# Performance work log

Measured on AMD Instinct MI355X. Metric: run time of the kernel, lower is better.

Reference implementation:

```python
import jax, jax.numpy as jnp
import numpy as np

H, D, HID, DIN = 2, 32, 64, 128
NQ, NA, NK = 100000, 200000, 200000
E_KQ, E_QK, E_QA, E_AQ = 800000, 800000, 400000, 400000
EP, EN = 100000, 100000


def setup_inputs() -> dict:
    key = jax.random.key(0)
    ks = jax.random.split(key, 32)
    f = lambda i, shape, s=0.05: jax.random.normal(ks[i], shape, dtype=jnp.float32) * s
    ri = lambda i, n, hi: jax.random.randint(ks[i], (n,), 0, hi)
    return {
        'xq': f(0, (NQ, DIN), 1.0), 'xa': f(1, (NA, DIN), 1.0), 'xk': f(2, (NK, DIN), 1.0),
        'lin_w': f(3, (3, DIN, HID)), 'lin_b': f(4, (3, HID)),
        'k_w': f(5, (3, HID, HID)), 'k_b': f(6, (3, HID)),
        'q_w': f(7, (3, HID, HID)), 'q_b': f(8, (3, HID)),
        'v_w': f(9, (3, HID, HID)), 'v_b': f(10, (3, HID)),
        'a_w': f(11, (3, HID, HID)), 'a_b': f(12, (3, HID)),
        'a_rel': f(13, (4, H, D, D), 0.2), 'm_rel': f(14, (4, H, D, D), 0.2),
        'p_rel': jnp.ones((4, H), dtype=jnp.float32),  # PyG init: ones
        'skip': jnp.ones((3,), dtype=jnp.float32),     # PyG init: ones
        'ei_kq_src': ri(15, E_KQ, NK), 'ei_kq_dst': ri(16, E_KQ, NQ),
        'ei_qk_src': ri(17, E_QK, NQ), 'ei_qk_dst': ri(18, E_QK, NA * 0 + NK),
        'ei_qa_src': ri(19, E_QA, NQ), 'ei_qa_dst': ri(20, E_QA, NA),
        'ei_aq_src': ri(21, E_AQ, NA), 'ei_aq_dst': ri(22, E_AQ, NQ),
        'pos_src': ri(23, EP, NQ), 'pos_dst': ri(24, EP, NA),
        'neg_src': ri(25, EN, NQ), 'neg_dst': ri(26, EN, NA),
    }


def _seg_softmax(alpha, dst, n):
    # softmax over incoming edges per destination node (per head)
    m = jax.ops.segment_max(alpha, dst, num_segments=n)
    m = jnp.where(jnp.isfinite(m), m, 0.0)
    e = jnp.exp(alpha - m[dst])
    s = jax.ops.segment_sum(e, dst, num_segments=n)
    return e / (s[dst] + 1e-16)


def hgt_forward(xq, xa, xk, lin_w, lin_b, k_w, k_b, q_w, q_b, v_w, v_b, a_w, a_b,
                a_rel, m_rel, p_rel, skip, edges):
    # node types: 0=question, 1=answer, 2=knowledge
    xs = [jax.nn.relu(x @ lin_w[i] + lin_b[i]) for i, x in enumerate([xq, xa, xk])]
    ns = [x.shape[0] for x in xs]
    k = [(x @ k_w[i] + k_b[i]).reshape(-1, H, D) for i, x in enumerate(xs)]
    q = [(x @ q_w[i] + q_b[i]).reshape(-1, H, D) for i, x in enumerate(xs)]
    v = [(x @ v_w[i] + v_b[i]).reshape(-1, H, D) for i, x in enumerate(xs)]
    out = [jnp.zeros((n, H, D), dtype=xs[0].dtype) for n in ns]
    scale = 1.0 / jnp.sqrt(jnp.float32(D))
    for st, dt, r, es, ed in edges:
        # per-edge-type head-wise key/value transforms (applied at node level)
        k_rel = jnp.einsum('nhd,hde->nhe', k[st], a_rel[r])
        v_rel = jnp.einsum('nhd,hde->nhe', v[st], m_rel[r])
        alpha = (q[dt][ed] * k_rel[es]).sum(-1) * p_rel[r] * scale  # [E,H]
        a = _seg_softmax(alpha, ed, ns[dt])
        msg = a[:, :, None] * v_rel[es]  # [E,H,D]
        out[dt] = out[dt] + jax.ops.segment_sum(msg, ed, num_segments=ns[dt])
    z = []
    for i in range(3):
        o = jax.nn.gelu(out[i].reshape(-1, H * D), approximate=False) @ a_w[i] + a_b[i]
        beta = jax.nn.sigmoid(skip[i])
        z.append(beta * o + (1.0 - beta) * xs[i])
    return z  # [z_question, z_answer, z_knowledge]; note: HGT.forward never applies self.lin


def reference(xq, xa, xk, lin_w, lin_b, k_w, k_b, q_w, q_b, v_w, v_b, a_w, a_b,
              a_rel, m_rel, p_rel, skip,
              ei_kq_src, ei_kq_dst, ei_qk_src, ei_qk_dst, ei_qa_src, ei_qa_dst,
              ei_aq_src, ei_aq_dst, pos_src, pos_dst, neg_src, neg_dst):
    edges = [
        (2, 0, 0, ei_kq_src, ei_kq_dst),  # knowledge -> question
        (0, 2, 1, ei_qk_src, ei_qk_dst),  # question -> knowledge
        (0, 1, 2, ei_qa_src, ei_qa_dst),  # question -> answer
        (1, 0, 3, ei_aq_src, ei_aq_dst),  # answer -> question
    ]
    zq, za, zk = hgt_forward(xq, xa, xk, lin_w, lin_b, k_w, k_b, q_w, q_b, v_w, v_b,
                             a_w, a_b, a_rel, m_rel, p_rel, skip, edges)
    pos_pred = jax.nn.sigmoid((zq[pos_src] * za[pos_dst]).sum(-1))
    neg_pred = jax.nn.sigmoid((zq[neg_src] * za[neg_dst]).sum(-1))
    return (pos_pred, neg_pred, zq, za, zk)
```

## Files before the change

### kernel.cpp

```cpp
#include <hip/hip_runtime.h>
#include <math.h>

namespace {

constexpr int NQn = 100000, NAn = 200000, NKn = 200000;
constexpr int EPc = 100000, ENc = 100000;
constexpr int ETOT = 2400000, NSEG = 600000;

constexpr long XSB_OFF  = 0;
constexpr long OUTB_OFF = 16000000;
constexpr long QBF_OFF  = 32000000;
constexpr long KV_OFF   = 48000000;
constexpr long ZB_OFF   = 86500000;
constexpr long WTB_OFF  = 96200000;
constexpr long WFB_OFF  = 96250000;
constexpr long INT_OFF  = 96300000;
constexpr long DEG_I  = 0;
constexpr long CUR_I  = 600000;
constexpr long OFFS_I = 1200000;
constexpr long PART_I = 1800064;
constexpr long CSRC_I = 1801088;

constexpr int LINT_U = 0;
constexpr int QT_U   = 24576;
constexpr int AT_U   = 36864;
constexpr int WFT_U  = 49152;

__constant__ long c_rbase[4] = {0, 200000, 300032, 400064};

typedef __attribute__((ext_vector_type(8))) short bf16x8;
typedef __attribute__((ext_vector_type(4))) float f32x4;

__device__ inline f32x4 mfma16(bf16x8 a, bf16x8 b, f32x4 c) {
    return __builtin_amdgcn_mfma_f32_16x16x32_bf16(a, b, c, 0, 0, 0);
}

__device__ inline float gelu_f(float x) {
    return 0.5f * x * (1.0f + erff(x * 0.7071067811865475f));
}
__device__ inline float bf2f(unsigned short u) {
    return __uint_as_float(((unsigned)u) << 16);
}
__device__ inline unsigned short f2bf(float f) {
    unsigned u = __float_as_uint(f);
    return (unsigned short)((u + 0x7fffu + ((u >> 16) & 1u)) >> 16);
}

__device__ inline void type_of_block128(int b, int& t, int& n0) {
    if (b < 782)       { t = 0; n0 = b * 128; }
    else if (b < 2345) { t = 1; n0 = (b - 782) * 128; }
    else               { t = 2; n0 = (b - 2345) * 128; }
}
__device__ inline void type_of_block64(int b, int& t, int& n0) {
    if (b < 1563)      { t = 0; n0 = b * 64; }
    else if (b < 4688) { t = 1; n0 = (b - 1563) * 64; }
    else               { t = 2; n0 = (b - 4688) * 64; }
}

template<int K>
__device__ inline void stage_bf16(unsigned short* lds, const unsigned short* src,
                                  int n0, int n, int tid)
{
    constexpr int CPR = K / 8;
    for (int c = tid; c < 128 * CPR; c += 256) {
        int row = c / CPR, kc = c % CPR;
        int node = n0 + row; if (node > n - 1) node = n - 1;
        uint4 v = *(const uint4*)&src[(long)node * K + kc * 8];
        int byte = (row * K + kc * 8) * 2;
        *(uint4*)((char*)lds + (byte ^ ((row & 7) << 4))) = v;
    }
}

__device__ inline void stage_out_gelu(unsigned short* lds, const unsigned short* src,
                                      int n0, int n, int tid)
{
    for (int c = tid; c < 128 * 8; c += 256) {
        int row = c >> 3, kc = c & 7;
        int node = n0 + row; if (node > n - 1) node = n - 1;
        uint4 v = *(const uint4*)&src[(long)node * 64 + kc * 8];
        float f0 = gelu_f(bf2f((unsigned short)(v.x & 0xffffu)));
        float f1 = gelu_f(bf2f((unsigned short)(v.x >> 16)));
        float f2 = gelu_f(bf2f((unsigned short)(v.y & 0xffffu)));
        float f3 = gelu_f(bf2f((unsigned short)(v.y >> 16)));
        float f4 = gelu_f(bf2f((unsigned short)(v.z & 0xffffu)));
        float f5 = gelu_f(bf2f((unsigned short)(v.z >> 16)));
        float f6 = gelu_f(bf2f((unsigned short)(v.w & 0xffffu)));
        float f7 = gelu_f(bf2f((unsigned short)(v.w >> 16)));
        uint4 o;
        o.x = (unsigned)f2bf(f0) | ((unsigned)f2bf(f1) << 16);
        o.y = (unsigned)f2bf(f2) | ((unsigned)f2bf(f3) << 16);
        o.z = (unsigned)f2bf(f4) | ((unsigned)f2bf(f5) << 16);
        o.w = (unsigned)f2bf(f6) | ((unsigned)f2bf(f7) << 16);
        int byte = (row * 64 + kc * 8) * 2;
        *(uint4*)((char*)lds + (byte ^ ((row & 7) << 4))) = o;
    }
}

template<int K, int ROWS>
__device__ inline void stage_f32(unsigned short* lds, const float* src,
                                 int n0, int n, int tid)
{
    constexpr int CPR = K / 8;
    for (int c = tid; c < ROWS * CPR; c += 256) {
        int row = c / CPR, kc = c % CPR;
        int node = n0 + row; if (node > n - 1) node = n - 1;
        const float* sp = &src[(long)node * K + kc * 8];
        float4 f0 = *(const float4*)sp, f1 = *(const float4*)(sp + 4);
        uint4 v;
        v.x = (unsigned)f2bf(f0.x) | ((unsigned)f2bf(f0.y) << 16);
        v.y = (unsigned)f2bf(f0.z) | ((unsigned)f2bf(f0.w) << 16);
        v.z = (unsigned)f2bf(f1.x) | ((unsigned)f2bf(f1.y) << 16);
        v.w = (unsigned)f2bf(f1.z) | ((unsigned)f2bf(f1.w) << 16);
        int byte = (row * K + kc * 8) * 2;
        *(uint4*)((char*)lds + (byte ^ ((row & 7) << 4))) = v;
    }
}

template<int N, int K>
__device__ inline void stage_w(unsigned short* lds, const unsigned short* wt, int tid)
{
    constexpr int CPR = K / 8;
    for (int c = tid; c < N * CPR; c += 256) {
        int nr = c / CPR, kc = c % CPR;
        uint4 v = *(const uint4*)&wt[nr * K + kc * 8];
        int byte = (nr * K + kc * 8) * 2;
        *(uint4*)((char*)lds + (byte ^ ((nr & 7) << 4))) = v;
    }
}

template<int K, int NF, int MF>
__device__ inline void mfma_coreT(const unsigned short* ldsX, const unsigned short* ldsW,
                                  f32x4 (&acc)[MF][NF], int lane, int w)
{
    const int lrow = lane & 15, lk = (lane >> 4) * 8;
    #pragma unroll
    for (int ks = 0; ks < K / 32; ++ks) {
        bf16x8 a[MF], b[NF];
        #pragma unroll
        for (int mf = 0; mf < MF; ++mf) {
            int row = w * (16 * MF) + mf * 16 + lrow;
            int byte = (row * K + ks * 32 + lk) * 2;
            a[mf] = *(const bf16x8*)((const char*)ldsX + (byte ^ ((row & 7) << 4)));
        }
        #pragma unroll
        for (int nf = 0; nf < NF; ++nf) {
            int nr = nf * 16 + lrow;
            int byte = (nr * K + ks * 32 + lk) * 2;
            b[nf] = *(const bf16x8*)((const char*)ldsW + (byte ^ ((nr & 7) << 4)));
        }
        #pragma unroll
        for (int mf = 0; mf < MF; ++mf)
            #pragma unroll
            for (int nf = 0; nf < NF; ++nf)
                acc[mf][nf] = mfma16(b[nf], a[mf], acc[mf][nf]);
    }
}

__global__ void prep_count(const float* __restrict__ lin_w, const float* __restrict__ q_w,
                           const float* __restrict__ a_w,
                           const float* __restrict__ kw, const float* __restrict__ kb,
                           const float* __restrict__ vw, const float* __restrict__ vb,
                           const float* __restrict__ a_rel, const float* __restrict__ m_rel,
                           unsigned short* __restrict__ wtb, float* __restrict__ wfb,
                           const int* __restrict__ d0, const int* __restrict__ d1,
                           const int* __restrict__ d2, const int* __restrict__ d3,
                           int* __restrict__ deg)
{
    const int tid = threadIdx.x;
    if (blockIdx.x < 4) {
        const int r = blockIdx.x;
        const int st_tab[4] = {2, 0, 0, 1};
        const int st = st_tab[r];
        for (int idx = tid; idx < 8192; idx += 256) {
            int d = idx >> 7, c = idx & 127;
            int i = c >> 1, which = c & 1;
            int h = i >> 5, e = i & 31;
            const float* w   = (which ? vw : kw) + st * 4096;
            const float* rel = (which ? m_rel : a_rel) + r * 2048;
            float s = 0.f;
            #pragma unroll
            for (int c32 = 0; c32 < 32; ++c32)
                s += w[d * 64 + h * 32 + c32] * rel[h * 1024 + c32 * 32 + e];
            wtb[WFT_U + r * 8192 + c * 64 + d] = f2bf(s);
        }
        for (int idx = tid; idx < 128; idx += 256) {
            int i = idx >> 1, which = idx & 1;
            int h = i >> 5, e = i & 31;
            const float* b   = (which ? vb : kb) + st * 64;
            const float* rel = (which ? m_rel : a_rel) + r * 2048;
            float s = 0.f;
            #pragma unroll
            for (int c32 = 0; c32 < 32; ++c32)
                s += b[h * 32 + c32] * rel[h * 1024 + c32 * 32 + e];
            wfb[r * 128 + idx] = s;
        }
    } else if (blockIdx.x < 196) {
        int i = (blockIdx.x - 4) * 256 + tid;
        if (i < 24576) {
            int t = i / 8192, rem = i % 8192, nn = rem >> 7, kk = rem & 127;
            wtb[LINT_U + i] = f2bf(lin_w[t * 8192 + kk * 64 + nn]);
        } else if (i < 36864) {
            int j = i - 24576;
            int t = j / 4096, rem = j % 4096, nn = rem >> 6, kk = rem & 63;
            wtb[QT_U + j] = f2bf(q_w[t * 4096 + kk * 64 + nn]);
        } else if (i < 49152) {
            int j = i - 36864;
            int t = j / 4096, rem = j % 4096, nn = rem >> 6, kk = rem & 63;
            wtb[AT_U + j] = f2bf(a_w[t * 4096 + kk * 64 + nn]);
        }
    } else {
        int gid = (blockIdx.x - 196) * 256 + tid;
        if (gid < 800000)       atomicAdd(&deg[d0[gid]], 1);
        else if (gid < 1600000) atomicAdd(&deg[100000 + d1[gid - 800000]], 1);
        else if (gid < 2000000) atomicAdd(&deg[300000 + d2[gid - 1600000]], 1);
        else if (gid < 2400000) atomicAdd(&deg[500000 + d3[gid - 2000000]], 1);
    }
}

__device__ inline void edge_map(int gid,
                                const int* __restrict__ s0, const int* __restrict__ d0,
                                const int* __restrict__ s1, const int* __restrict__ d1,
                                const int* __restrict__ s2, const int* __restrict__ d2,
                                const int* __restrict__ s3, const int* __restrict__ d3,
                                int& seg, int& s)
{
    if (gid < 800000)       { seg = d0[gid];                    s = s0[gid]; }
    else if (gid < 1600000) { seg = 100000 + d1[gid - 800000];  s = s1[gid - 800000]; }
    else if (gid < 2000000) { seg = 300000 + d2[gid - 1600000]; s = s2[gid - 1600000]; }
    else                    { seg = 500000 + d3[gid - 2000000]; s = s3[gid - 2000000]; }
}

__global__ void __launch_bounds__(256)
fill_lin(const int* __restrict__ s0, const int* __restrict__ d0,
         const int* __restrict__ s1, const int* __restrict__ d1,
         const int* __restrict__ s2, const int* __restrict__ d2,
         const int* __restrict__ s3, const int* __restrict__ d3,
         const int* __restrict__ off, int* __restrict__ cur, int* __restrict__ csrc,
         const float* __restrict__ xq, const float* __restrict__ xa,
         const float* __restrict__ xk, const unsigned short* __restrict__ wtb,
         const float* __restrict__ lin_b, unsigned short* __restrict__ xsb)
{
    __shared__ unsigned short ldsX[64 * 128];
    __shared__ unsigned short ldsW[64 * 128];
    const int b = blockIdx.x;
    const int tid = threadIdx.x;

    int linb, fillb;
    if (b < 9376) {
        if (b & 1) { fillb = b >> 1; linb = -1; }
        else       { linb = b >> 1;  fillb = -1; }
    } else { linb = 4688 + (b - 9376); fillb = -1; }

    if (fillb >= 0) {
        int base = fillb * 256 + tid;
        if (base < 1200000) {
            int segA, sA, segB, sB;
            edge_map(base,           s0, d0, s1, d1, s2, d2, s3, d3, segA, sA);
            edge_map(base + 1200000, s0, d0, s1, d1, s2, d2, s3, d3, segB, sB);
            int oA = off[segA], oB = off[segB];
            int slotA = oA + atomicAdd(&cur[segA], 1);
            int slotB = oB + atomicAdd(&cur[segB], 1);
            csrc[slotA] = sA;
            csrc[slotB] = sB;
        }
        return;
    }

    int t, n0; type_of_block64(linb, t, n0);
    const int cnt[3] = {NQn, NAn, NKn};
    const long noff[3] = {0, NQn, NQn + NAn};
    const float* X = (t == 0) ? xq : (t == 1) ? xa : xk;
    const int n = cnt[t];

    stage_w<64, 128>(ldsW, wtb + LINT_U + t * 8192, tid);
    stage_f32<128, 64>(ldsX, X, n0, n, tid);
    __syncthreads();

    const int w = tid >> 6, lane = tid & 63;
    f32x4 acc[1][4] = {};
    mfma_coreT<128, 4, 1>(ldsX, ldsW, acc, lane, w);

    const int nodeL = lane & 15, colG = (lane >> 4) * 4;
    int node = n0 + w * 16 + nodeL;
    if (node < n) {
        #pragma unroll
        for (int nf = 0; nf < 4; ++nf) {
            int col0 = nf * 16 + colG;
            float4 bv = *(const float4*)&lin_b[t * 64 + col0];
            ushort4 o;
            o.x = f2bf(fmaxf(acc[0][nf][0] + bv.x, 0.f));
            o.y = f2bf(fmaxf(acc[0][nf][1] + bv.y, 0.f));
            o.z = f2bf(fmaxf(acc[0][nf][2] + bv.z, 0.f));
            o.w = f2bf(fmaxf(acc[0][nf][3] + bv.w, 0.f));
            *(ushort4*)&xsb[(noff[t] + node) * 64 + col0] = o;
        }
    }
}

__global__ void __launch_bounds__(256)
qkv_split(const unsigned short* __restrict__ xsb, const unsigned short* __restrict__ wtb,
          const float* __restrict__ q_b, const float* __restrict__ wfb,
          unsigned short* __restrict__ qbf, unsigned short* __restrict__ kvb)
{
    __shared__ unsigned short ldsX[128 * 64];
    __shared__ unsigned short ldsW[128 * 64];
    const int cnt[3] = {NQn, NAn, NKn};
    const long noff[3] = {0, NQn, NQn + NAn};
    const int tid = threadIdx.x;
    const int w = tid >> 6, lane = tid & 63;
    const int nodeL = lane & 15, colG = (lane >> 4) * 4;
    const int b = blockIdx.x;

    if (b < 3908) {
        int t, n0; type_of_block128(b, t, n0);
        const int n = cnt[t];
        stage_bf16<64>(ldsX, xsb + noff[t] * 64, n0, n, tid);
        stage_w<64, 64>(ldsW, wtb + QT_U + t * 4096, tid);
        __syncthreads();

        f32x4 acc[2][4] = {};
        mfma_coreT<64, 4, 2>(ldsX, ldsW, acc, lane, w);
        #pragma unroll
        for (int mf = 0; mf < 2; ++mf) {
            int node = n0 + w * 32 + mf * 16 + nodeL;
            if (node < n) {
                #pragma unroll
                for (int nf = 0; nf < 4; ++nf) {
                    int col0 = nf * 16 + colG;
                    float4 bv = *(const float4*)&q_b[t * 64 + col0];
                    ushort4 o;
                    o.x = f2bf(acc[mf][nf][0] + bv.x);
                    o.y = f2bf(acc[mf][nf][1] + bv.y);
                    o.z = f2bf(acc[mf][nf][2] + bv.z);
                    o.w = f2bf(acc[mf][nf][3] + bv.w);
                    *(ushort4*)&qbf[(noff[t] + node) * 64 + col0] = o;
                }
            }
        }
    } else {
        int kb = b - 3908, r, lb;
        if (kb < 1563)      { r = 0; lb = kb; }
        else if (kb < 2345) { r = 1; lb = kb - 1563; }
        else if (kb < 3127) { r = 2; lb = kb - 2345; }
        else                { r = 3; lb = kb - 3127; }
        const int stt[4] = {2, 0, 0, 1};
        const int st = stt[r];
        const int n0 = lb * 128;
        const int n = cnt[st];
        const long rb = c_rbase[r];

        stage_bf16<64>(ldsX, xsb + noff[st] * 64, n0, n, tid);
        stage_w<128, 64>(ldsW, wtb + WFT_U + r * 8192, tid);
        __syncthreads();

        f32x4 acc[2][8] = {};
        mfma_coreT<64, 8, 2>(ldsX, ldsW, acc, lane, w);
        #pragma unroll
        for (int mf = 0; mf < 2; ++mf) {
            int node = n0 + w * 32 + mf * 16 + nodeL;
            if (node < n) {
                #pragma unroll
                for (int nf = 0; nf < 8; ++nf) {
                    int col0 = nf * 16 + colG;
                    float4 bv = *(const float4*)&wfb[r * 128 + col0];
                    ushort4 o;
                    o.x = f2bf(acc[mf][nf][0] + bv.x);
                    o.y = f2bf(acc[mf][nf][1] + bv.y);
                    o.z = f2bf(acc[mf][nf][2] + bv.z);
                    o.w = f2bf(acc[mf][nf][3] + bv.w);
                    *(ushort4*)&kvb[(rb + node) * 128 + col0] = o;
                }
            }
        }
    }
}

__global__ void __launch_bounds__(256)
head_mfma(const unsigned short* __restrict__ outb, const unsigned short* __restrict__ xsb,
          const unsigned short* __restrict__ wtb, const float* __restrict__ a_b,
          const float* __restrict__ skip, float* __restrict__ z,
          unsigned short* __restrict__ zb)
{
    __shared__ unsigned short ldsX[128 * 64];
    __shared__ unsigned short ldsW[64 * 64];
    int t, n0; type_of_block128(blockIdx.x, t, n0);
    const int cnt[3] = {NQn, NAn, NKn};
    const long noff[3] = {0, NQn, NQn + NAn};
    const long zoff[3] = {200000L, 6600000L, 19400000L};
    const int n = cnt[t];
    const int tid = threadIdx.x;

    stage_w<64, 64>(ldsW, wtb + AT_U + t * 4096, tid);
    stage_out_gelu(ldsX, outb + noff[t] * 64, n0, n, tid);
    __syncthreads();

    const int w = tid >> 6, lane = tid & 63;
    f32x4 acc[2][4] = {};
    mfma_coreT<64, 4, 2>(ldsX, ldsW, acc, lane, w);

    const float beta = 1.f / (1.f + expf(-skip[t]));
    const int nodeL = lane & 15, colG = (lane >> 4) * 4;
    #pragma unroll
    for (int mf = 0; mf < 2; ++mf) {
        int node = n0 + w * 32 + mf * 16 + nodeL;
        if (node < n) {
            #pragma unroll
            for (int nf = 0; nf < 4; ++nf) {
                int col0 = nf * 16 + colG;
                float4 bv = *(const float4*)&a_b[t * 64 + col0];
                ushort4 rv = *(const ushort4*)&xsb[(noff[t] + node) * 64 + col0];
                float4 o;
                o.x = beta * (acc[mf][nf][0] + bv.x) + (1.f - beta) * bf2f(rv.x);
                o.y = beta * (acc[mf][nf][1] + bv.y) + (1.f - beta) * bf2f(rv.y);
                o.z = beta * (acc[mf][nf][2] + bv.z) + (1.f - beta) * bf2f(rv.z);
                o.w = beta * (acc[mf][nf][3] + bv.w) + (1.f - beta) * bf2f(rv.w);
                *(float4*)&z[zoff[t] + (long)node * 64 + col0] = o;
                if (t < 2) {
                    ushort4 p;
                    p.x = f2bf(o.x); p.y = f2bf(o.y); p.z = f2bf(o.z); p.w = f2bf(o.w);
                    long zrow = (t == 0) ? (long)node : 100000L + node;
                    *(ushort4*)&zb[zrow * 64 + col0] = p;
                }
            }
        }
    }
}

__global__ void scan1(const int* __restrict__ in, int* __restrict__ out,
                      int* __restrict__ part, int n)
{
    __shared__ int lds[256];
    const int tid = threadIdx.x;
    const int base = blockIdx.x * 1024 + tid * 4;
    int v[4];
    #pragma unroll
    for (int k = 0; k < 4; ++k) v[k] = (base + k < n) ? in[base + k] : 0;
    int tsum = v[0] + v[1] + v[2] + v[3];
    lds[tid] = tsum;
    __syncthreads();
    for (int off = 1; off < 256; off <<= 1) {
        int t = (tid >= off) ? lds[tid - off] : 0;
        __syncthreads();
        lds[tid] += t;
        __syncthreads();
    }
    int excl = lds[tid] - tsum;
    #pragma unroll
    for (int k = 0; k < 4; ++k) {
        if (base + k < n) out[base + k] = excl;
        excl += v[k];
    }
    if (tid == 255) part[blockIdx.x] = lds[255];
}

__global__ void scan2(int* __restrict__ part, int nb)
{
    __shared__ int lds[256];
    const int tid = threadIdx.x;
    const int base = tid * 4;
    int v[4];
    #pragma unroll
    for (int k = 0; k < 4; ++k) v[k] = (base + k < nb) ? part[base + k] : 0;
    int tsum = v[0] + v[1] + v[2] + v[3];
    lds[tid] = tsum;
    __syncthreads();
    for (int off = 1; off < 256; off <<= 1) {
        int t = (tid >= off) ? lds[tid - off] : 0;
        __syncthreads();
        lds[tid] += t;
        __syncthreads();
    }
    int excl = lds[tid] - tsum;
    #pragma unroll
    for (int k = 0; k < 4; ++k) {
        if (base + k < nb) part[base + k] = excl;
        excl += v[k];
    }
}

__global__ void scan3(int* __restrict__ off, const int* __restrict__ part, int n, int E)
{
    int i = blockIdx.x * 256 + threadIdx.x;
    if (i < n) off[i] += part[i >> 10];
    if (i == 0) off[n] = E;
}

__device__ inline void attn_node(const int* __restrict__ csrc, int begin, int end,
                                 const unsigned short* __restrict__ kvt,
                                 const float qv[4], int j, float res[4])
{
    float ss = 0.f, a0 = 0.f, a1 = 0.f, a2 = 0.f, a3 = 0.f;

    for (int t = begin; t < end; t += 4) {
        bool v1 = (t + 1 < end), v2 = (t + 2 < end), v3 = (t + 3 < end);
        int s0 = csrc[t];
        int s1 = csrc[v1 ? t + 1 : t];
        int s2 = csrc[v2 ? t + 2 : t];
        int s3 = csrc[v3 ? t + 3 : t];
        uint4 k0 = *(const uint4*)(kvt + (long)s0 * 128 + j * 8);
        uint4 k1 = *(const uint4*)(kvt + (long)s1 * 128 + j * 8);
        uint4 k2 = *(const uint4*)(kvt + (long)s2 * 128 + j * 8);
        uint4 k3 = *(const uint4*)(kvt + (long)s3 * 128 + j * 8);

        float p0 = __uint_as_float(k0.x << 16) * qv[0] + __uint_as_float(k0.y << 16) * qv[1]
                 + __uint_as_float(k0.z << 16) * qv[2] + __uint_as_float(k0.w << 16) * qv[3];
        float p1 = __uint_as_float(k1.x << 16) * qv[0] + __uint_as_float(k1.y << 16) * qv[1]
                 + __uint_as_float(k1.z << 16) * qv[2] + __uint_as_float(k1.w << 16) * qv[3];
        float p2 = __uint_as_float(k2.x << 16) * qv[0] + __uint_as_float(k2.y << 16) * qv[1]
                 + __uint_as_float(k2.z << 16) * qv[2] + __uint_as_float(k2.w << 16) * qv[3];
        float p3 = __uint_as_float(k3.x << 16) * qv[0] + __uint_as_float(k3.y << 16) * qv[1]
                 + __uint_as_float(k3.z << 16) * qv[2] + __uint_as_float(k3.w << 16) * qv[3];

        p0 += __shfl_xor(p0, 1);  p1 += __shfl_xor(p1, 1);
        p2 += __shfl_xor(p2, 1);  p3 += __shfl_xor(p3, 1);
        p0 += __shfl_xor(p0, 2);  p1 += __shfl_xor(p1, 2);
        p2 += __shfl_xor(p2, 2);  p3 += __shfl_xor(p3, 2);
        p0 += __shfl_xor(p0, 4);  p1 += __shfl_xor(p1, 4);
        p2 += __shfl_xor(p2, 4);  p3 += __shfl_xor(p3, 4);

        float w0 = exp2f(fminf(p0, 115.f));
        float w1 = v1 ? exp2f(fminf(p1, 115.f)) : 0.f;
        float w2 = v2 ? exp2f(fminf(p2, 115.f)) : 0.f;
        float w3 = v3 ? exp2f(fminf(p3, 115.f)) : 0.f;

        ss += (w0 + w1) + (w2 + w3);
        a0 += w0 * __uint_as_float(k0.x & 0xffff0000u) + w1 * __uint_as_float(k1.x & 0xffff0000u)
            + w2 * __uint_as_float(k2.x & 0xffff0000u) + w3 * __uint_as_float(k3.x & 0xffff0000u);
        a1 += w0 * __uint_as_float(k0.y & 0xffff0000u) + w1 * __uint_as_float(k1.y & 0xffff0000u)
            + w2 * __uint_as_float(k2.y & 0xffff0000u) + w3 * __uint_as_float(k3.y & 0xffff0000u);
        a2 += w0 * __uint_as_float(k0.z & 0xffff0000u) + w1 * __uint_as_float(k1.z & 0xffff0000u)
            + w2 * __uint_as_float(k2.z & 0xffff0000u) + w3 * __uint_as_float(k3.z & 0xffff0000u);
        a3 += w0 * __uint_as_float(k0.w & 0xffff0000u) + w1 * __uint_as_float(k1.w & 0xffff0000u)
            + w2 * __uint_as_float(k2.w & 0xffff0000u) + w3 * __uint_as_float(k3.w & 0xffff0000u);
    }

    float inv = 1.f / (ss + 1e-16f);
    res[0] = a0 * inv; res[1] = a1 * inv; res[2] = a2 * inv; res[3] = a3 * inv;
}

__global__ void __launch_bounds__(256)
attn_all(const int* __restrict__ off, const int* __restrict__ csrc,
         const unsigned short* __restrict__ qbf, const unsigned short* __restrict__ kv,
         const float* __restrict__ prel, float scale, unsigned short* __restrict__ outb)
{
    const int tid = threadIdx.x;
    const int nid = blockIdx.x * 16 + (tid >> 4);
    const int j = tid & 15;
    const int h = j >> 3;
    const float l2e = 1.4426950408889634f;

    long row; int segA, segB = -1; long kbA, kbB = 0; float psA, psB = 0.f;
    if (nid < 100000) {
        row = nid;
        segA = nid;            kbA = c_rbase[0]; psA = prel[0 + h] * scale * l2e;
        segB = 500000 + nid;   kbB = c_rbase[3]; psB = prel[6 + h] * scale * l2e;
    } else if (nid < 300000) {
        int kk = nid - 100000;
        row = 300000 + kk;
        segA = 100000 + kk;    kbA = c_rbase[1]; psA = prel[2 + h] * scale * l2e;
    } else {
        int aa = nid - 300000;
        row = 100000 + aa;
        segA = 300000 + aa;    kbA = c_rbase[2]; psA = prel[4 + h] * scale * l2e;
    }

    ushort4 q4 = *(const ushort4*)&qbf[row * 64 + 4 * j];
    float qraw[4] = {bf2f(q4.x), bf2f(q4.y), bf2f(q4.z), bf2f(q4.w)};

    float res[4];
    {
        float qv[4] = {qraw[0] * psA, qraw[1] * psA, qraw[2] * psA, qraw[3] * psA};
        attn_node(csrc, off[segA], off[segA + 1], kv + kbA * 128, qv, j, res);
    }
    if (segB >= 0) {
        float qv[4] = {qraw[0] * psB, qraw[1] * psB, qraw[2] * psB, qraw[3] * psB};
        float r2[4];
        attn_node(csrc, off[segB], off[segB + 1], kv + kbB * 128, qv, j, r2);
        res[0] += r2[0]; res[1] += r2[1]; res[2] += r2[2]; res[3] += r2[3];
    }

    ushort4 o;
    o.x = f2bf(res[0]); o.y = f2bf(res[1]); o.z = f2bf(res[2]); o.w = f2bf(res[3]);
    *(ushort4*)&outb[row * 64 + 4 * j] = o;
}

__global__ void pred_all(const int* __restrict__ psrc, const int* __restrict__ pdst,
                         const int* __restrict__ nsrc, const int* __restrict__ ndst,
                         const unsigned short* __restrict__ zb, float* __restrict__ out)
{
    int t = blockIdx.x * 256 + threadIdx.x;
    int g = t >> 3, lane = t & 7;
    if (g >= EPc + ENc) return;
    int s, d;
    if (g < EPc) { s = psrc[g]; d = pdst[g]; }
    else         { int gg = g - EPc; s = nsrc[gg]; d = ndst[gg]; }
    uint4 zs = *(const uint4*)&zb[(long)s * 64 + lane * 8];
    uint4 zd = *(const uint4*)&zb[(100000L + d) * 64 + lane * 8];
    float p = 0.f;
    p += bf2f((unsigned short)(zs.x & 0xffffu)) * bf2f((unsigned short)(zd.x & 0xffffu));
    p += bf2f((unsigned short)(zs.x >> 16))     * bf2f((unsigned short)(zd.x >> 16));
    p += bf2f((unsigned short)(zs.y & 0xffffu)) * bf2f((unsigned short)(zd.y & 0xffffu));
    p += bf2f((unsigned short)(zs.y >> 16))     * bf2f((unsigned short)(zd.y >> 16));
    p += bf2f((unsigned short)(zs.z & 0xffffu)) * bf2f((unsigned short)(zd.z & 0xffffu));
    p += bf2f((unsigned short)(zs.z >> 16))     * bf2f((unsigned short)(zd.z >> 16));
    p += bf2f((unsigned short)(zs.w & 0xffffu)) * bf2f((unsigned short)(zd.w & 0xffffu));
    p += bf2f((unsigned short)(zs.w >> 16))     * bf2f((unsigned short)(zd.w >> 16));
    p += __shfl_xor(p, 1);
    p += __shfl_xor(p, 2);
    p += __shfl_xor(p, 4);
    if (lane == 0) out[g] = 1.f / (1.f + expf(-p));
}

}

extern "C" void kernel_launch(void* const* d_in, const int* in_sizes, int n_in,
                              void* d_out, int out_size, void* d_ws, size_t ws_size,
                              hipStream_t stream)
{
    const float* xq    = (const float*)d_in[0];
    const float* xa    = (const float*)d_in[1];
    const float* xk    = (const float*)d_in[2];
    const float* lin_w = (const float*)d_in[3];
    const float* lin_b = (const float*)d_in[4];
    const float* k_w   = (const float*)d_in[5];
    const float* k_b   = (const float*)d_in[6];
    const float* q_w   = (const float*)d_in[7];
    const float* q_b   = (const float*)d_in[8];
    const float* v_w   = (const float*)d_in[9];
    const float* v_b   = (const float*)d_in[10];
    const float* a_w   = (const float*)d_in[11];
    const float* a_b   = (const float*)d_in[12];
    const float* a_rel = (const float*)d_in[13];
    const float* m_rel = (const float*)d_in[14];
    const float* p_rel = (const float*)d_in[15];
    const float* skip  = (const float*)d_in[16];
    const int* esrc[4] = {(const int*)d_in[17], (const int*)d_in[19], (const int*)d_in[21], (const int*)d_in[23]};
    const int* edst[4] = {(const int*)d_in[18], (const int*)d_in[20], (const int*)d_in[22], (const int*)d_in[24]};
    const int* pos_src = (const int*)d_in[25];
    const int* pos_dst = (const int*)d_in[26];
    const int* neg_src = (const int*)d_in[27];
    const int* neg_dst = (const int*)d_in[28];

    float* ws   = (float*)d_ws;
    float* outp = (float*)d_out;
    int*   wi   = (int*)(ws + INT_OFF);
    unsigned short* xsb  = (unsigned short*)(ws + XSB_OFF);
    unsigned short* outb = (unsigned short*)(ws + OUTB_OFF);
    unsigned short* qbf  = (unsigned short*)(ws + QBF_OFF);
    unsigned short* kvb  = (unsigned short*)(ws + KV_OFF);
    unsigned short* zbb  = (unsigned short*)(ws + ZB_OFF);
    unsigned short* wtb  = (unsigned short*)(ws + WTB_OFF);
    float*          wfb  = ws + WFB_OFF;

    hipMemsetAsync(wi + DEG_I, 0, 1200000L * sizeof(int), stream);

    prep_count<<<196 + 9375, 256, 0, stream>>>(
        lin_w, q_w, a_w, k_w, k_b, v_w, v_b, a_rel, m_rel, wtb, wfb,
        edst[0], edst[1], edst[2], edst[3], wi + DEG_I);

    const int nb = (NSEG + 1023) / 1024;
    scan1<<<nb, 256, 0, stream>>>(wi + DEG_I, wi + OFFS_I, wi + PART_I, NSEG);
    scan2<<<1, 256, 0, stream>>>(wi + PART_I, nb);
    scan3<<<(NSEG + 255) / 256, 256, 0, stream>>>(wi + OFFS_I, wi + PART_I, NSEG, ETOT);

    fill_lin<<<12501, 256, 0, stream>>>(
        esrc[0], edst[0], esrc[1], edst[1], esrc[2], edst[2], esrc[3], edst[3],
        wi + OFFS_I, wi + CUR_I, wi + CSRC_I,
        xq, xa, xk, wtb, lin_b, xsb);

    qkv_split<<<8598, 256, 0, stream>>>(xsb, wtb, q_b, wfb, qbf, kvb);

    const float scale = 0.17677669529663687f;
    attn_all<<<31250, 256, 0, stream>>>(wi + OFFS_I, wi + CSRC_I, qbf, kvb,
                                        p_rel, scale, outb);

    head_mfma<<<3908, 256, 0, stream>>>(outb, xsb, wtb, a_b, skip, outp, zbb);

    pred_all<<<(200000 * 8 + 255) / 256, 256, 0, stream>>>(
        pos_src, pos_dst, neg_src, neg_dst, zbb, outp);
}
```

Measured before the change: 594.1 us.

## Move input linear into prep/degree-count kernel and merge QKV with CSR fill

The input projection (linear+ReLU) now runs inside the first kernel alongside weight prep and degree counting, and stages lin_w directly from fp32 with an in-LDS transpose instead of using a pre-converted bf16 copy. The CSR fill is now interleaved with the QKV projection blocks in one launch, removing one kernel launch and letting the gather-heavy fill overlap with compute. The cost is that every linear block converts lin_w itself with scalar LDS stores, and block scheduling and occupancy now depend on how the mixed workloads share each launch.

Result: slower. 635.2 us (+6.9%).

```diff
diff --git a/kernel.cpp b/kernel.cpp
--- a/kernel.cpp
+++ b/kernel.cpp
@@ -21,10 +21,9 @@
 constexpr long PART_I = 1800064;
 constexpr long CSRC_I = 1801088;
 
-constexpr int LINT_U = 0;
-constexpr int QT_U   = 24576;
-constexpr int AT_U   = 36864;
-constexpr int WFT_U  = 49152;
+constexpr int QT_U   = 0;
+constexpr int AT_U   = 12288;
+constexpr int WFT_U  = 24576;
 
 __constant__ long c_rbase[4] = {0, 200000, 300032, 400064};
 
@@ -128,6 +127,21 @@
     }
 }
 
+__device__ inline void stage_wT_f32(unsigned short* lds, const float* w, int tid)
+{
+    for (int c = tid * 4; c < 8192; c += 1024) {
+        int kk = c >> 6, nn0 = c & 63;
+        float4 v = *(const float4*)&w[kk * 64 + nn0];
+        float vals[4] = {v.x, v.y, v.z, v.w};
+        #pragma unroll
+        for (int i = 0; i < 4; ++i) {
+            int nn = nn0 + i;
+            int byte = (nn * 128 + kk) * 2;
+            *(unsigned short*)((char*)lds + (byte ^ ((nn & 7) << 4))) = f2bf(vals[i]);
+        }
+    }
+}
+
 template<int K, int NF, int MF>
 __device__ inline void mfma_coreT(const unsigned short* ldsX, const unsigned short* ldsW,
                                   f32x4 (&acc)[MF][NF], int lane, int w)
@@ -156,19 +170,69 @@
     }
 }
 
-__global__ void prep_count(const float* __restrict__ lin_w, const float* __restrict__ q_w,
-                           const float* __restrict__ a_w,
-                           const float* __restrict__ kw, const float* __restrict__ kb,
-                           const float* __restrict__ vw, const float* __restrict__ vb,
-                           const float* __restrict__ a_rel, const float* __restrict__ m_rel,
-                           unsigned short* __restrict__ wtb, float* __restrict__ wfb,
-                           const int* __restrict__ d0, const int* __restrict__ d1,
-                           const int* __restrict__ d2, const int* __restrict__ d3,
-                           int* __restrict__ deg)
-{
+__device__ inline void edge_map(int gid,
+                                const int* __restrict__ s0, const int* __restrict__ d0,
+                                const int* __restrict__ s1, const int* __restrict__ d1,
+                                const int* __restrict__ s2, const int* __restrict__ d2,
+                                const int* __restrict__ s3, const int* __restrict__ d3,
+                                int& seg, int& s)
+{
+    if (gid < 800000)       { seg = d0[gid];                    s = s0[gid]; }
+    else if (gid < 1600000) { seg = 100000 + d1[gid - 800000];  s = s1[gid - 800000]; }
+    else if (gid < 2000000) { seg = 300000 + d2[gid - 1600000]; s = s2[gid - 1600000]; }
+    else                    { seg = 500000 + d3[gid - 2000000]; s = s3[gid - 2000000]; }
+}
+
+__global__ void __launch_bounds__(256)
+lin_prep_count(const float* __restrict__ xq, const float* __restrict__ xa,
+               const float* __restrict__ xk, const float* __restrict__ lin_w,
+               const float* __restrict__ lin_b, unsigned short* __restrict__ xsb,
+               const float* __restrict__ q_w, const float* __restrict__ a_w,
+               const float* __restrict__ kw, const float* __restrict__ kb,
+               const float* __restrict__ vw, const float* __restrict__ vb,
+               const float* __restrict__ a_rel, const float* __restrict__ m_rel,
+               unsigned short* __restrict__ wtb, float* __restrict__ wfb,
+               const int* __restrict__ d0, const int* __restrict__ d1,
+               const int* __restrict__ d2, const int* __restrict__ d3,
+               int* __restrict__ deg)
+{
+    __shared__ unsigned short ldsX[64 * 128];
+    __shared__ unsigned short ldsW[64 * 128];
+    const int b = blockIdx.x;
     const int tid = threadIdx.x;
-    if (blockIdx.x < 4) {
-        const int r = blockIdx.x;
+
+    if (b < 7813) {
+        int t, n0; type_of_block64(b, t, n0);
+        const int cnt[3] = {NQn, NAn, NKn};
+        const long noff[3] = {0, NQn, NQn + NAn};
+        const float* X = (t == 0) ? xq : (t == 1) ? xa : xk;
+        const int n = cnt[t];
+
+        stage_wT_f32(ldsW, lin_w + (long)t * 8192, tid);
+        stage_f32<128, 64>(ldsX, X, n0, n, tid);
+        __syncthreads();
+
+        const int w = tid >> 6, lane = tid & 63;
+        f32x4 acc[1][4] = {};
+        mfma_coreT<128, 4, 1>(ldsX, ldsW, acc, lane, w);
+
+        const int nodeL = lane & 15, colG = (lane >> 4) * 4;
+        int node = n0 + w * 16 + nodeL;
+        if (node < n) {
+            #pragma unroll
+            for (int nf = 0; nf < 4; ++nf) {
+                int col0 = nf * 16 + colG;
+                float4 bv = *(const float4*)&lin_b[t * 64 + col0];
+                ushort4 o;
+                o.x = f2bf(fmaxf(acc[0][nf][0] + bv.x, 0.f));
+                o.y = f2bf(fmaxf(acc[0][nf][1] + bv.y, 0.f));
+                o.z = f2bf(fmaxf(acc[0][nf][2] + bv.z, 0.f));
+                o.w = f2bf(fmaxf(acc[0][nf][3] + bv.w, 0.f));
+                *(ushort4*)&xsb[(noff[t] + node) * 64 + col0] = o;
+            }
+        }
+    } else if (b < 7817) {
+        const int r = b - 7813;
         const int st_tab[4] = {2, 0, 0, 1};
         const int st = st_tab[r];
         for (int idx = tid; idx < 8192; idx += 256) {
@@ -186,30 +250,26 @@
         for (int idx = tid; idx < 128; idx += 256) {
             int i = idx >> 1, which = idx & 1;
             int h = i >> 5, e = i & 31;
-            const float* b   = (which ? vb : kb) + st * 64;
+            const float* bb  = (which ? vb : kb) + st * 64;
             const float* rel = (which ? m_rel : a_rel) + r * 2048;
             float s = 0.f;
             #pragma unroll
             for (int c32 = 0; c32 < 32; ++c32)
-                s += b[h * 32 + c32] * rel[h * 1024 + c32 * 32 + e];
+                s += bb[h * 32 + c32] * rel[h * 1024 + c32 * 32 + e];
             wfb[r * 128 + idx] = s;
         }
-    } else if (blockIdx.x < 196) {
-        int i = (blockIdx.x - 4) * 256 + tid;
-        if (i < 24576) {
-            int t = i / 8192, rem = i % 8192, nn = rem >> 7, kk = rem & 127;
-            wtb[LINT_U + i] = f2bf(lin_w[t * 8192 + kk * 64 + nn]);
-        } else if (i < 36864) {
-            int j = i - 24576;
-            int t = j / 4096, rem = j % 4096, nn = rem >> 6, kk = rem & 63;
-            wtb[QT_U + j] = f2bf(q_w[t * 4096 + kk * 64 + nn]);
-        } else if (i < 49152) {
-            int j = i - 36864;
+    } else if (b < 7913) {
+        int i = (b - 7817) * 256 + tid;
+        if (i < 12288) {
+            int t = i / 4096, rem = i % 4096, nn = rem >> 6, kk = rem & 63;
+            wtb[QT_U + i] = f2bf(q_w[t * 4096 + kk * 64 + nn]);
+        } else {
+            int j = i - 12288;
             int t = j / 4096, rem = j % 4096, nn = rem >> 6, kk = rem & 63;
             wtb[AT_U + j] = f2bf(a_w[t * 4096 + kk * 64 + nn]);
         }
     } else {
-        int gid = (blockIdx.x - 196) * 256 + tid;
+        int gid = (b - 7913) * 256 + tid;
         if (gid < 800000)       atomicAdd(&deg[d0[gid]], 1);
         else if (gid < 1600000) atomicAdd(&deg[100000 + d1[gid - 800000]], 1);
         else if (gid < 2000000) atomicAdd(&deg[300000 + d2[gid - 1600000]], 1);
@@ -217,39 +277,26 @@
     }
 }
 
-__device__ inline void edge_map(int gid,
-                                const int* __restrict__ s0, const int* __restrict__ d0,
-                                const int* __restrict__ s1, const int* __restrict__ d1,
-                                const int* __restrict__ s2, const int* __restrict__ d2,
-                                const int* __restrict__ s3, const int* __restrict__ d3,
-                                int& seg, int& s)
-{
-    if (gid < 800000)       { seg = d0[gid];                    s = s0[gid]; }
-    else if (gid < 1600000) { seg = 100000 + d1[gid - 800000];  s = s1[gid - 800000]; }
-    else if (gid < 2000000) { seg = 300000 + d2[gid - 1600000]; s = s2[gid - 1600000]; }
-    else                    { seg = 500000 + d3[gid - 2000000]; s = s3[gid - 2000000]; }
-}
-
 __global__ void __launch_bounds__(256)
-fill_lin(const int* __restrict__ s0, const int* __restrict__ d0,
+fill_qkv(const int* __restrict__ s0, const int* __restrict__ d0,
          const int* __restrict__ s1, const int* __restrict__ d1,
          const int* __restrict__ s2, const int* __restrict__ d2,
          const int* __restrict__ s3, const int* __restrict__ d3,
          const int* __restrict__ off, int* __restrict__ cur, int* __restrict__ csrc,
-         const float* __restrict__ xq, const float* __restrict__ xa,
-         const float* __restrict__ xk, const unsigned short* __restrict__ wtb,
-         const float* __restrict__ lin_b, unsigned short* __restrict__ xsb)
-{
-    __shared__ unsigned short ldsX[64 * 128];
-    __shared__ unsigned short ldsW[64 * 128];
+         const unsigned short* __restrict__ xsb, const unsigned short* __restrict__ wtb,
+         const float* __restrict__ q_b, const float* __restrict__ wfb,
+         unsigned short* __restrict__ qbf, unsigned short* __restrict__ kvb)
+{
+    __shared__ unsigned short ldsX[128 * 64];
+    __shared__ unsigned short ldsW[128 * 64];
     const int b = blockIdx.x;
     const int tid = threadIdx.x;
 
-    int linb, fillb;
+    int qkvb, fillb;
     if (b < 9376) {
-        if (b & 1) { fillb = b >> 1; linb = -1; }
-        else       { linb = b >> 1;  fillb = -1; }
-    } else { linb = 4688 + (b - 9376); fillb = -1; }
+        if (b & 1) { fillb = b >> 1; qkvb = -1; }
+        else       { qkvb = b >> 1;  fillb = -1; }
+    } else { qkvb = 4688 + (b - 9376); fillb = -1; }
 
     if (fillb >= 0) {
         int base = fillb * 256 + tid;
@@ -266,53 +313,13 @@
         return;
     }
 
-    int t, n0; type_of_block64(linb, t, n0);
     const int cnt[3] = {NQn, NAn, NKn};
     const long noff[3] = {0, NQn, NQn + NAn};
-    const float* X = (t == 0) ? xq : (t == 1) ? xa : xk;
-    const int n = cnt[t];
-
-    stage_w<64, 128>(ldsW, wtb + LINT_U + t * 8192, tid);
-    stage_f32<128, 64>(ldsX, X, n0, n, tid);
-    __syncthreads();
-
-    const int w = tid >> 6, lane = tid & 63;
-    f32x4 acc[1][4] = {};
-    mfma_coreT<128, 4, 1>(ldsX, ldsW, acc, lane, w);
-
-    const int nodeL = lane & 15, colG = (lane >> 4) * 4;
-    int node = n0 + w * 16 + nodeL;
-    if (node < n) {
-        #pragma unroll
-        for (int nf = 0; nf < 4; ++nf) {
-            int col0 = nf * 16 + colG;
-            float4 bv = *(const float4*)&lin_b[t * 64 + col0];
-            ushort4 o;
-            o.x = f2bf(fmaxf(acc[0][nf][0] + bv.x, 0.f));
-            o.y = f2bf(fmaxf(acc[0][nf][1] + bv.y, 0.f));
-            o.z = f2bf(fmaxf(acc[0][nf][2] + bv.z, 0.f));
-            o.w = f2bf(fmaxf(acc[0][nf][3] + bv.w, 0.f));
-            *(ushort4*)&xsb[(noff[t] + node) * 64 + col0] = o;
-        }
-    }
-}
-
-__global__ void __launch_bounds__(256)
-qkv_split(const unsigned short* __restrict__ xsb, const unsigned short* __restrict__ wtb,
-          const float* __restrict__ q_b, const float* __restrict__ wfb,
-          unsigned short* __restrict__ qbf, unsigned short* __restrict__ kvb)
-{
-    __shared__ unsigned short ldsX[128 * 64];
-    __shared__ unsigned short ldsW[128 * 64];
-    const int cnt[3] = {NQn, NAn, NKn};
-    const long noff[3] = {0, NQn, NQn + NAn};
-    const int tid = threadIdx.x;
     const int w = tid >> 6, lane = tid & 63;
     const int nodeL = lane & 15, colG = (lane >> 4) * 4;
-    const int b = blockIdx.x;
-
-    if (b < 3908) {
-        int t, n0; type_of_block128(b, t, n0);
+
+    if (qkvb < 3908) {
+        int t, n0; type_of_block128(qkvb, t, n0);
         const int n = cnt[t];
         stage_bf16<64>(ldsX, xsb + noff[t] * 64, n0, n, tid);
         stage_w<64, 64>(ldsW, wtb + QT_U + t * 4096, tid);
@@ -338,7 +345,7 @@
             }
         }
     } else {
-        int kb = b - 3908, r, lb;
+        int kb = qkvb - 3908, r, lb;
         if (kb < 1563)      { r = 0; lb = kb; }
         else if (kb < 2345) { r = 1; lb = kb - 1563; }
         else if (kb < 3127) { r = 2; lb = kb - 2345; }
@@ -654,8 +661,9 @@
 
     hipMemsetAsync(wi + DEG_I, 0, 1200000L * sizeof(int), stream);
 
-    prep_count<<<196 + 9375, 256, 0, stream>>>(
-        lin_w, q_w, a_w, k_w, k_b, v_w, v_b, a_rel, m_rel, wtb, wfb,
+    lin_prep_count<<<7913 + 9375, 256, 0, stream>>>(
+        xq, xa, xk, lin_w, lin_b, xsb,
+        q_w, a_w, k_w, k_b, v_w, v_b, a_rel, m_rel, wtb, wfb,
         edst[0], edst[1], edst[2], edst[3], wi + DEG_I);
 
     const int nb = (NSEG + 1023) / 1024;
@@ -663,12 +671,10 @@
     scan2<<<1, 256, 0, stream>>>(wi + PART_I, nb);
     scan3<<<(NSEG + 255) / 256, 256, 0, stream>>>(wi + OFFS_I, wi + PART_I, NSEG, ETOT);
 
-    fill_lin<<<12501, 256, 0, stream>>>(
+    fill_qkv<<<13286, 256, 0, stream>>>(
         esrc[0], edst[0], esrc[1], edst[1], esrc[2], edst[2], esrc[3], edst[3],
         wi + OFFS_I, wi + CUR_I, wi + CSRC_I,
-        xq, xa, xk, wtb, lin_b, xsb);
-
-    qkv_split<<<8598, 256, 0, stream>>>(xsb, wtb, q_b, wfb, qbf, kvb);
+        xsb, wtb, q_b, wfb, qbf, kvb);
 
     const float scale = 0.17677669529663687f;
     attn_all<<<31250, 256, 0, stream>>>(wi + OFFS_I, wi + CSRC_I, qbf, kvb,
```

## Record per-edge rank during degree count to drop second atomic pass in CSR fill

Applied to the files above, without the earlier changes.

The degree-counting kernel now stores the value returned by each atomicAdd as that edge's rank within its destination segment. The CSR fill can then write each source index directly to offset plus rank, with no second atomic pass over a cursor array. The fill work is folded into every linear-projection block (two edges per thread) instead of alternating separate fill blocks, which shrinks the grid. This costs an extra 2.4M-int rank array that must be written and read back, but removes the cursor memset and the atomic contention in the fill. CSR order within a segment is now fixed by the count pass, so the sum order in the segment softmax can differ slightly.

Result: faster. 549.0 us (-7.6%).

```diff
diff --git a/kernel.cpp b/kernel.cpp
--- a/kernel.cpp
+++ b/kernel.cpp
@@ -6,6 +6,7 @@
 constexpr int NQn = 100000, NAn = 200000, NKn = 200000;
 constexpr int EPc = 100000, ENc = 100000;
 constexpr int ETOT = 2400000, NSEG = 600000;
+constexpr int LIN_THREADS = 7813 * 256;
 
 constexpr long XSB_OFF  = 0;
 constexpr long OUTB_OFF = 16000000;
@@ -16,10 +17,10 @@
 constexpr long WFB_OFF  = 96250000;
 constexpr long INT_OFF  = 96300000;
 constexpr long DEG_I  = 0;
-constexpr long CUR_I  = 600000;
-constexpr long OFFS_I = 1200000;
-constexpr long PART_I = 1800064;
-constexpr long CSRC_I = 1801088;
+constexpr long OFFS_I = 600064;
+constexpr long PART_I = 1200128;
+constexpr long RANK_I = 1201152;
+constexpr long CSRC_I = 3601152;
 
 constexpr int LINT_U = 0;
 constexpr int QT_U   = 24576;
@@ -156,6 +157,28 @@
     }
 }
 
+__device__ inline void edge_map(int gid,
+                                const int* __restrict__ s0, const int* __restrict__ d0,
+                                const int* __restrict__ s1, const int* __restrict__ d1,
+                                const int* __restrict__ s2, const int* __restrict__ d2,
+                                const int* __restrict__ s3, const int* __restrict__ d3,
+                                int& seg, int& s)
+{
+    if (gid < 800000)       { seg = d0[gid];                    s = s0[gid]; }
+    else if (gid < 1600000) { seg = 100000 + d1[gid - 800000];  s = s1[gid - 800000]; }
+    else if (gid < 2000000) { seg = 300000 + d2[gid - 1600000]; s = s2[gid - 1600000]; }
+    else                    { seg = 500000 + d3[gid - 2000000]; s = s3[gid - 2000000]; }
+}
+__device__ inline int edge_seg(int gid,
+                               const int* __restrict__ d0, const int* __restrict__ d1,
+                               const int* __restrict__ d2, const int* __restrict__ d3)
+{
+    if (gid < 800000)       return d0[gid];
+    else if (gid < 1600000) return 100000 + d1[gid - 800000];
+    else if (gid < 2000000) return 300000 + d2[gid - 1600000];
+    else                    return 500000 + d3[gid - 2000000];
+}
+
 __global__ void prep_count(const float* __restrict__ lin_w, const float* __restrict__ q_w,
                            const float* __restrict__ a_w,
                            const float* __restrict__ kw, const float* __restrict__ kb,
@@ -164,7 +187,7 @@
                            unsigned short* __restrict__ wtb, float* __restrict__ wfb,
                            const int* __restrict__ d0, const int* __restrict__ d1,
                            const int* __restrict__ d2, const int* __restrict__ d3,
-                           int* __restrict__ deg)
+                           int* __restrict__ deg, int* __restrict__ rank)
 {
     const int tid = threadIdx.x;
     if (blockIdx.x < 4) {
@@ -210,63 +233,43 @@
         }
     } else {
         int gid = (blockIdx.x - 196) * 256 + tid;
-        if (gid < 800000)       atomicAdd(&deg[d0[gid]], 1);
-        else if (gid < 1600000) atomicAdd(&deg[100000 + d1[gid - 800000]], 1);
-        else if (gid < 2000000) atomicAdd(&deg[300000 + d2[gid - 1600000]], 1);
-        else if (gid < 2400000) atomicAdd(&deg[500000 + d3[gid - 2000000]], 1);
-    }
-}
-
-__device__ inline void edge_map(int gid,
-                                const int* __restrict__ s0, const int* __restrict__ d0,
-                                const int* __restrict__ s1, const int* __restrict__ d1,
-                                const int* __restrict__ s2, const int* __restrict__ d2,
-                                const int* __restrict__ s3, const int* __restrict__ d3,
-                                int& seg, int& s)
-{
-    if (gid < 800000)       { seg = d0[gid];                    s = s0[gid]; }
-    else if (gid < 1600000) { seg = 100000 + d1[gid - 800000];  s = s1[gid - 800000]; }
-    else if (gid < 2000000) { seg = 300000 + d2[gid - 1600000]; s = s2[gid - 1600000]; }
-    else                    { seg = 500000 + d3[gid - 2000000]; s = s3[gid - 2000000]; }
+        if (gid < ETOT) {
+            int seg = edge_seg(gid, d0, d1, d2, d3);
+            rank[gid] = atomicAdd(&deg[seg], 1);
+        }
+    }
 }
 
 __global__ void __launch_bounds__(256)
-fill_lin(const int* __restrict__ s0, const int* __restrict__ d0,
+lin_fill(const int* __restrict__ s0, const int* __restrict__ d0,
          const int* __restrict__ s1, const int* __restrict__ d1,
          const int* __restrict__ s2, const int* __restrict__ d2,
          const int* __restrict__ s3, const int* __restrict__ d3,
-         const int* __restrict__ off, int* __restrict__ cur, int* __restrict__ csrc,
+         const int* __restrict__ off, const int* __restrict__ rank,
+         int* __restrict__ csrc,
          const float* __restrict__ xq, const float* __restrict__ xa,
          const float* __restrict__ xk, const unsigned short* __restrict__ wtb,
          const float* __restrict__ lin_b, unsigned short* __restrict__ xsb)
 {
     __shared__ unsigned short ldsX[64 * 128];
     __shared__ unsigned short ldsW[64 * 128];
-    const int b = blockIdx.x;
     const int tid = threadIdx.x;
-
-    int linb, fillb;
-    if (b < 9376) {
-        if (b & 1) { fillb = b >> 1; linb = -1; }
-        else       { linb = b >> 1;  fillb = -1; }
-    } else { linb = 4688 + (b - 9376); fillb = -1; }
-
-    if (fillb >= 0) {
-        int base = fillb * 256 + tid;
-        if (base < 1200000) {
-            int segA, sA, segB, sB;
-            edge_map(base,           s0, d0, s1, d1, s2, d2, s3, d3, segA, sA);
-            edge_map(base + 1200000, s0, d0, s1, d1, s2, d2, s3, d3, segB, sB);
-            int oA = off[segA], oB = off[segB];
-            int slotA = oA + atomicAdd(&cur[segA], 1);
-            int slotB = oB + atomicAdd(&cur[segB], 1);
-            csrc[slotA] = sA;
-            csrc[slotB] = sB;
-        }
-        return;
-    }
-
-    int t, n0; type_of_block64(linb, t, n0);
+    const int gid = blockIdx.x * 256 + tid;
+
+    int segA, sA;
+    edge_map(gid, s0, d0, s1, d1, s2, d2, s3, d3, segA, sA);
+    int rkA = rank[gid];
+    int offA = off[segA];
+    const int gidB = gid + LIN_THREADS;
+    const bool hasB = gidB < ETOT;
+    int segB = 0, sB = 0, rkB = 0, offB = 0;
+    if (hasB) {
+        edge_map(gidB, s0, d0, s1, d1, s2, d2, s3, d3, segB, sB);
+        rkB = rank[gidB];
+        offB = off[segB];
+    }
+
+    int t, n0; type_of_block64(blockIdx.x, t, n0);
     const int cnt[3] = {NQn, NAn, NKn};
     const long noff[3] = {0, NQn, NQn + NAn};
     const float* X = (t == 0) ? xq : (t == 1) ? xa : xk;
@@ -275,6 +278,9 @@
     stage_w<64, 128>(ldsW, wtb + LINT_U + t * 8192, tid);
     stage_f32<128, 64>(ldsX, X, n0, n, tid);
     __syncthreads();
+
+    csrc[offA + rkA] = sA;
+    if (hasB) csrc[offB + rkB] = sB;
 
     const int w = tid >> 6, lane = tid & 63;
     f32x4 acc[1][4] = {};
@@ -652,20 +658,20 @@
     unsigned short* wtb  = (unsigned short*)(ws + WTB_OFF);
     float*          wfb  = ws + WFB_OFF;
 
-    hipMemsetAsync(wi + DEG_I, 0, 1200000L * sizeof(int), stream);
+    hipMemsetAsync(wi + DEG_I, 0, 600000L * sizeof(int), stream);
 
     prep_count<<<196 + 9375, 256, 0, stream>>>(
         lin_w, q_w, a_w, k_w, k_b, v_w, v_b, a_rel, m_rel, wtb, wfb,
-        edst[0], edst[1], edst[2], edst[3], wi + DEG_I);
+        edst[0], edst[1], edst[2], edst[3], wi + DEG_I, wi + RANK_I);
 
     const int nb = (NSEG + 1023) / 1024;
     scan1<<<nb, 256, 0, stream>>>(wi + DEG_I, wi + OFFS_I, wi + PART_I, NSEG);
     scan2<<<1, 256, 0, stream>>>(wi + PART_I, nb);
     scan3<<<(NSEG + 255) / 256, 256, 0, stream>>>(wi + OFFS_I, wi + PART_I, NSEG, ETOT);
 
-    fill_lin<<<12501, 256, 0, stream>>>(
+    lin_fill<<<7813, 256, 0, stream>>>(
         esrc[0], edst[0], esrc[1], edst[1], esrc[2], edst[2], esrc[3], edst[3],
-        wi + OFFS_I, wi + CUR_I, wi + CSRC_I,
+        wi + OFFS_I, wi + RANK_I, wi + CSRC_I,
         xq, xa, xk, wtb, lin_b, xsb);
 
     qkv_split<<<8598, 256, 0, stream>>>(xsb, wtb, q_b, wfb, qbf, kvb);
```
